# Kernel optimization log

Measured on AMD Instinct MI355X. Metric: run time of the kernel, lower is better.

Reference implementation:

```python
import jax, jax.numpy as jnp
import numpy as np

N = 50000      # query points
N0 = 50000     # support points
M = 32         # neighbors per query
K = 15         # kernel points
DIM = 3
D_IN = 64
D_OUT = 64
POINT_INFLUENCE = 1.0
KERNEL_RADIUS = 1.5 * POINT_INFLUENCE  # _INFLUENCE_TO_RADIUS * point_influence


def setup_inputs() -> dict:
    key = jax.random.key(0)
    k1, k2, k3, k4, k5 = jax.random.split(key, 5)
    query_points = jax.random.normal(k1, (N, DIM), jnp.float32)
    support_points = jax.random.normal(k2, (N0, DIM), jnp.float32)
    neighbors = jax.random.randint(k3, (N, M), 0, N0 + 1)  # index N0 = shadow point
    x = jax.random.normal(k4, (N0, D_IN), jnp.float32)
    # Kernel point dispositions: fixed center point, rest spread within kernel radius
    # (stand-in for kernel_point_optimization_debug; K_points is a frozen parameter).
    rng = np.random.RandomState(0)
    kp = rng.uniform(-1.0, 1.0, (K, DIM))
    kp[0, :] = 0.0
    kp = kp * (KERNEL_RADIUS / np.max(np.linalg.norm(kp, axis=1)))
    K_points = jnp.asarray(kp, dtype=jnp.float32)
    # Xavier-normal conv weights [K, D_IN, D_OUT]
    std = (2.0 / (D_IN + D_OUT)) ** 0.5
    weight = jax.random.normal(k5, (K, D_IN, D_OUT), jnp.float32) * std
    return {
        "query_points": query_points,
        "support_points": support_points,
        "neighbors": neighbors,
        "x": x,
        "K_points": K_points,
        "weight": weight,
    }


def reference(query_points, support_points, neighbors, x, K_points, weight):
    # Shadow support point far away + zero shadow feature row
    shadow = jnp.full((1, query_points.shape[1]), 1e6, dtype=support_points.dtype)
    sp = jnp.concatenate([support_points, shadow], axis=0)            # [N0+1, 3]
    xp = jnp.concatenate([x, jnp.zeros((1, x.shape[1]), x.dtype)], axis=0)  # [N0+1, d]

    # Gather neighbor coords, center on query point
    neighb_pts = sp[neighbors] - query_points[:, None, :]             # [N, M, 3]
    # Squared distances to each kernel point
    diff = neighb_pts[:, :, None, :] - K_points[None, None, :, :]     # [N, M, K, 3]
    sq_distances = jnp.sum(diff * diff, axis=-1)                      # [N, M, K]

    # Linear influence, then transpose to [N, K, M]
    all_weights = jnp.clip(1.0 - jnp.sqrt(sq_distances) / POINT_INFLUENCE, 0.0)
    all_weights = jnp.swapaxes(all_weights, 1, 2)                     # [N, K, M]

    # Gather neighbor features and aggregate per kernel point
    feats = xp[neighbors]                                             # [N, M, d]
    weighted = jnp.einsum("nkm,nmd->nkd", all_weights, feats)        # [N, K, d]
    # Apply per-kernel-point weight matrices and sum over kernel points
    out = jnp.einsum("nkd,kdo->no", weighted, weight)                # [N, out]
    return out
```

## Files before the change

### kernel.cpp

```cpp
#include <hip/hip_runtime.h>

#define NQ 50000
#define NS 50000
#define MNB 32
#define KP 15
#define QPB 32
#define NBLK 1563

typedef __bf16 bf16x8 __attribute__((ext_vector_type(8)));
typedef float  f32x4  __attribute__((ext_vector_type(4)));

__device__ __forceinline__ unsigned short bf1(float f) {
    union { __bf16 h; unsigned short s; } r; r.h = (__bf16)f; return r.s;
}
__device__ __forceinline__ unsigned pk2(float a, float b) {
    union { __bf16 h[2]; unsigned u; } r;
    r.h[0] = (__bf16)a; r.h[1] = (__bf16)b; return r.u;
}

#define PERM_LO 0x05040100u
#define PERM_HI 0x07060302u

__global__ __launch_bounds__(256) void conv_prep(const float* __restrict__ W,
                                                 uint4* __restrict__ wBf,
                                                 const float* __restrict__ x,
                                                 uint4* __restrict__ xBf) {
    const int b = blockIdx.x;
    if (b < 32) {
        const int c = b * 256 + threadIdx.x;
        const int cl = c & 15, qq = (c >> 4) & 3, ks = (c >> 6) & 31, cc = c >> 11;
        const int k0 = ks * 32 + qq * 8;
        const int o  = cc * 16 + cl;
        union { unsigned short s[8]; uint4 u; } pk;
        #pragma unroll
        for (int j = 0; j < 8; ++j)
            pk.s[j] = (k0 + j < KP * 64) ? bf1(W[(size_t)(k0 + j) * 64 + o])
                                         : (unsigned short)0;
        wBf[c] = pk.u;
    } else {
        const int t = (b - 32) * 256 + threadIdx.x;
        if (t < (NS * 64) / 8) {
            const float4* __restrict__ x4 = (const float4*)x;
            const float4 a = x4[t * 2];
            const float4 c2 = x4[t * 2 + 1];
            uint4 o;
            o.x = pk2(a.x, a.y);  o.y = pk2(a.z, a.w);
            o.z = pk2(c2.x, c2.y); o.w = pk2(c2.z, c2.w);
            xBf[t] = o;
        }
    }
}

__global__ __launch_bounds__(1024, 8) void kpconv_fused(
    const float* __restrict__ qp, const float* __restrict__ sp,
    const int* __restrict__ nb, const uint2* __restrict__ xb,
    const float* __restrict__ kpts, const uint4* __restrict__ wBf,
    float* __restrict__ out)
{
    __shared__ struct {
        __align__(16) unsigned short wt[QPB * 1024];
        union {
            float4 rc4[QPB][MNB];
            f32x4  red[8][64];
        } u;
    } sm;

    const int tid  = threadIdx.x;
    const int lane = tid & 63;
    const int wv   = __builtin_amdgcn_readfirstlane(tid >> 6);
    const int cl = lane & 15, q = lane >> 4;
    const int n0 = blockIdx.x * QPB;

    const int   kidx = (cl < KP) ? cl : (KP - 1);
    const float kx = kpts[kidx * 3 + 0];
    const float ky = kpts[kidx * 3 + 1];
    const float kz = kpts[kidx * 3 + 2];
    const float gate = (cl < KP) ? 1.0f : 0.0f;

    {
        const int m  = lane & 31, gh = lane >> 5;
        const int n  = n0 + wv * 2 + gh;
        float rx = 1e6f, ry = 1e6f, rz = 1e6f; int idc = 0;
        if (n < NQ) {
            const int id = nb[n * MNB + m];
            const float qx = qp[n * 3 + 0], qy = qp[n * 3 + 1], qz = qp[n * 3 + 2];
            float sx = 1e6f, sy = 1e6f, sz = 1e6f;
            if (id < NS) { sx = sp[id*3+0]; sy = sp[id*3+1]; sz = sp[id*3+2]; }
            rx = sx - qx; ry = sy - qy; rz = sz - qz;
            idc = (id < NS) ? id : 0;
        }
        sm.u.rc4[wv * 2 + gh][m] = (float4){rx, ry, rz, __int_as_float(idc)};
    }

    const f32x4 zero = (f32x4){0.f, 0.f, 0.f, 0.f};
    #pragma unroll 1
    for (int gg = 0; gg < 2; ++gg) {
        const int g = wv * 2 + gg;
        float w[8]; uint2 r[8];
        #pragma unroll
        for (int j = 0; j < 8; ++j) {
            const float4 rc = sm.u.rc4[g][4 * j + q];
            const float dx = rc.x - kx, dy = rc.y - ky, dz = rc.z - kz;
            const float d2 = dx * dx + dy * dy + dz * dz;
            w[j] = fmaxf(1.0f - __builtin_amdgcn_sqrtf(d2), 0.0f) * gate;
            r[j] = xb[(size_t)__float_as_uint(rc.w) * 16 + cl];
        }
        union { uint4 u; bf16x8 v; } wf;
        wf.u.x = pk2(w[0], w[1]); wf.u.y = pk2(w[2], w[3]);
        wf.u.z = pk2(w[4], w[5]); wf.u.w = pk2(w[6], w[7]);
        union { uint4 u; bf16x8 v; } af[4];
        #pragma unroll
        for (int pr = 0; pr < 4; ++pr) {
            const uint2 e = r[2 * pr], o = r[2 * pr + 1];
            ((unsigned*)&af[0].u)[pr] = __builtin_amdgcn_perm(o.x, e.x, PERM_LO);
            ((unsigned*)&af[1].u)[pr] = __builtin_amdgcn_perm(o.x, e.x, PERM_HI);
            ((unsigned*)&af[2].u)[pr] = __builtin_amdgcn_perm(o.y, e.y, PERM_LO);
            ((unsigned*)&af[3].u)[pr] = __builtin_amdgcn_perm(o.y, e.y, PERM_HI);
        }
        f32x4 acc[4];
        #pragma unroll
        for (int cb = 0; cb < 4; ++cb)
            acc[cb] = __builtin_amdgcn_mfma_f32_16x16x32_bf16(af[cb].v, wf.v, zero, 0, 0, 0);
        unsigned pkd[8];
        #pragma unroll
        for (int i = 0; i < 4; ++i) {
            pkd[2 * i]     = pk2(acc[0][i], acc[1][i]);
            pkd[2 * i + 1] = pk2(acc[2][i], acc[3][i]);
        }
        const unsigned key = (unsigned)(((g & 7) ^ (cl & 7)) << 4);
        char* base = (char*)sm.wt + g * 2048;
        const unsigned i0 = (unsigned)(cl * 128 + q * 32);
        *(uint4*)(base + ((i0)      ^ key)) = (uint4){pkd[0], pkd[1], pkd[2], pkd[3]};
        *(uint4*)(base + ((i0 + 16) ^ key)) = (uint4){pkd[4], pkd[5], pkd[6], pkd[7]};
    }

    __syncthreads();

    const int h  = wv >> 3;
    const int tl = wv & 7;
    const int rc = tl >> 2, cc = tl & 3;
    const char* abase = (const char*)sm.wt + (rc * 16 + cl) * 2048;
    const unsigned akey = (unsigned)((cl & 7) << 4);
    const uint4* wb = wBf + (((cc * 32 + h * 16) * 4 + q) * 16 + cl);
    f32x4 d0 = zero, d1 = zero;
    #pragma unroll 4
    for (int it = 0; it < 16; it += 2) {
        const int ks0 = h * 16 + it;
        const unsigned kk  = (unsigned)((((ks0 >> 1) & 7)) << 4);
        const unsigned ia0 = (unsigned)(ks0 * 64 + q * 16);
        const bf16x8 a0 = *(const bf16x8*)(abase + ((ia0)      ^ akey ^ kk));
        const bf16x8 a1 = *(const bf16x8*)(abase + ((ia0 + 64) ^ akey ^ kk));
        union { uint4 u; bf16x8 v; } b0, b1;
        b0.u = wb[it * 64];
        b1.u = wb[it * 64 + 64];
        d0 = __builtin_amdgcn_mfma_f32_16x16x32_bf16(a0, b0.v, d0, 0, 0, 0);
        d1 = __builtin_amdgcn_mfma_f32_16x16x32_bf16(a1, b1.v, d1, 0, 0, 0);
    }
    f32x4 dd = d0 + d1;
    if (h == 1) sm.u.red[tl][lane] = dd;
    __syncthreads();
    if (h == 0) {
        dd += sm.u.red[tl][lane];
        #pragma unroll
        for (int i = 0; i < 4; ++i) {
            const int n = n0 + rc * 16 + q * 4 + i;
            if (n < NQ) out[(size_t)n * 64 + cc * 16 + cl] = dd[i];
        }
    }
}

extern "C" void kernel_launch(void* const* d_in, const int* in_sizes, int n_in,
                              void* d_out, int out_size, void* d_ws, size_t ws_size,
                              hipStream_t stream) {
    const float* qp   = (const float*)d_in[0];
    const float* sp   = (const float*)d_in[1];
    const int*   nb   = (const int*)d_in[2];
    const float* x    = (const float*)d_in[3];
    const float* kpts = (const float*)d_in[4];
    const float* W    = (const float*)d_in[5];
    float* out = (float*)d_out;

    uint4* wBf = (uint4*)d_ws;
    uint4* xBf = (uint4*)((char*)d_ws + 131072);

    hipLaunchKernelGGL(conv_prep, dim3(32 + (NS * 64 / 8 + 255) / 256), dim3(256),
                       0, stream, W, wBf, x, xBf);
    hipLaunchKernelGGL(kpconv_fused, dim3(NBLK), dim3(1024), 0, stream,
                       qp, sp, nb, (const uint2*)xBf, kpts, wBf, out);
}
```

Before: 122.5 us.

## Pad shadow row in prep and gather neighbors directly without LDS staging

The prep kernel now writes padded copies of the support coordinates and bf16 features, with a shadow row at index NS (coordinates 1e6, features zero). The fused kernel can then gather coordinates and features straight from global memory per MFMA lane, with no shadow-index branch and no LDS staging of relative coordinates. Each lane now reloads coordinates and the neighbor index itself (redundantly across its 16 column lanes), and the query offset is folded into the kernel-point position. Nontemporal hints are added on the neighbor loads and output stores.

```diff
diff --git a/kernel.cpp b/kernel.cpp
--- a/kernel.cpp
+++ b/kernel.cpp
@@ -6,6 +6,10 @@
 #define KP 15
 #define QPB 32
 #define NBLK 1563
+
+#define WBF_BYTES 131072
+#define XBF_BYTES ((NS + 1) * 128)
+#define SP2_OFF   (WBF_BYTES + XBF_BYTES)
 
 typedef __bf16 bf16x8 __attribute__((ext_vector_type(8)));
 typedef float  f32x4  __attribute__((ext_vector_type(4)));
@@ -24,7 +28,9 @@
 __global__ __launch_bounds__(256) void conv_prep(const float* __restrict__ W,
                                                  uint4* __restrict__ wBf,
                                                  const float* __restrict__ x,
-                                                 uint4* __restrict__ xBf) {
+                                                 uint4* __restrict__ xBf,
+                                                 const float* __restrict__ sp,
+                                                 float* __restrict__ sp2) {
     const int b = blockIdx.x;
     if (b < 32) {
         const int c = b * 256 + threadIdx.x;
@@ -37,7 +43,7 @@
             pk.s[j] = (k0 + j < KP * 64) ? bf1(W[(size_t)(k0 + j) * 64 + o])
                                          : (unsigned short)0;
         wBf[c] = pk.u;
-    } else {
+    } else if (b < 1595) {
         const int t = (b - 32) * 256 + threadIdx.x;
         if (t < (NS * 64) / 8) {
             const float4* __restrict__ x4 = (const float4*)x;
@@ -47,22 +53,25 @@
             o.x = pk2(a.x, a.y);  o.y = pk2(a.z, a.w);
             o.z = pk2(c2.x, c2.y); o.w = pk2(c2.z, c2.w);
             xBf[t] = o;
+        } else if (t < (NS * 64) / 8 + 8) {
+            xBf[t] = (uint4){0u, 0u, 0u, 0u};
         }
+    } else {
+        const int i = (b - 1595) * 256 + threadIdx.x;
+        if (i < (NS + 1) * 3)
+            sp2[i] = (i < NS * 3) ? sp[i] : 1e6f;
     }
 }
 
 __global__ __launch_bounds__(1024, 8) void kpconv_fused(
-    const float* __restrict__ qp, const float* __restrict__ sp,
+    const float* __restrict__ qp, const float* __restrict__ sp2,
     const int* __restrict__ nb, const uint2* __restrict__ xb,
     const float* __restrict__ kpts, const uint4* __restrict__ wBf,
     float* __restrict__ out)
 {
     __shared__ struct {
         __align__(16) unsigned short wt[QPB * 1024];
-        union {
-            float4 rc4[QPB][MNB];
-            f32x4  red[8][64];
-        } u;
+        __align__(16) f32x4 red[8][64];
     } sm;
 
     const int tid  = threadIdx.x;
@@ -71,40 +80,37 @@
     const int cl = lane & 15, q = lane >> 4;
     const int n0 = blockIdx.x * QPB;
 
-    const int   kidx = (cl < KP) ? cl : (KP - 1);
-    const float kx = kpts[kidx * 3 + 0];
-    const float ky = kpts[kidx * 3 + 1];
-    const float kz = kpts[kidx * 3 + 2];
-    const float gate = (cl < KP) ? 1.0f : 0.0f;
-
-    {
-        const int m  = lane & 31, gh = lane >> 5;
-        const int n  = n0 + wv * 2 + gh;
-        float rx = 1e6f, ry = 1e6f, rz = 1e6f; int idc = 0;
-        if (n < NQ) {
-            const int id = nb[n * MNB + m];
-            const float qx = qp[n * 3 + 0], qy = qp[n * 3 + 1], qz = qp[n * 3 + 2];
-            float sx = 1e6f, sy = 1e6f, sz = 1e6f;
-            if (id < NS) { sx = sp[id*3+0]; sy = sp[id*3+1]; sz = sp[id*3+2]; }
-            rx = sx - qx; ry = sy - qy; rz = sz - qz;
-            idc = (id < NS) ? id : 0;
-        }
-        sm.u.rc4[wv * 2 + gh][m] = (float4){rx, ry, rz, __int_as_float(idc)};
-    }
+    const float kx = (cl < KP) ? kpts[cl * 3 + 0] : 1e9f;
+    const float ky = (cl < KP) ? kpts[cl * 3 + 1] : 1e9f;
+    const float kz = (cl < KP) ? kpts[cl * 3 + 2] : 1e9f;
 
     const f32x4 zero = (f32x4){0.f, 0.f, 0.f, 0.f};
+
     #pragma unroll 1
     for (int gg = 0; gg < 2; ++gg) {
         const int g = wv * 2 + gg;
+        const int n = n0 + g;
+        const int nc = (n < NQ) ? n : (NQ - 1);
+        const float qx = qp[nc * 3 + 0];
+        const float qy = qp[nc * 3 + 1];
+        const float qz = qp[nc * 3 + 2];
+        const float kqx = kx + qx, kqy = ky + qy, kqz = kz + qz;
+        const int* __restrict__ nbq = nb + nc * MNB;
+
         float w[8]; uint2 r[8];
         #pragma unroll
         for (int j = 0; j < 8; ++j) {
-            const float4 rc = sm.u.rc4[g][4 * j + q];
-            const float dx = rc.x - kx, dy = rc.y - ky, dz = rc.z - kz;
+            const unsigned id = (unsigned)__builtin_nontemporal_load(&nbq[4 * j + q]);
+            const unsigned so = id * 3u;
+            const float sx = sp2[so + 0];
+            const float sy = sp2[so + 1];
+            const float sz = sp2[so + 2];
+            r[j] = xb[id * 16u + (unsigned)cl];
+            const float dx = sx - kqx, dy = sy - kqy, dz = sz - kqz;
             const float d2 = dx * dx + dy * dy + dz * dz;
-            w[j] = fmaxf(1.0f - __builtin_amdgcn_sqrtf(d2), 0.0f) * gate;
-            r[j] = xb[(size_t)__float_as_uint(rc.w) * 16 + cl];
+            w[j] = fmaxf(1.0f - __builtin_amdgcn_sqrtf(d2), 0.0f);
         }
+
         union { uint4 u; bf16x8 v; } wf;
         wf.u.x = pk2(w[0], w[1]); wf.u.y = pk2(w[2], w[3]);
         wf.u.z = pk2(w[4], w[5]); wf.u.w = pk2(w[6], w[7]);
@@ -157,14 +163,15 @@
         d1 = __builtin_amdgcn_mfma_f32_16x16x32_bf16(a1, b1.v, d1, 0, 0, 0);
     }
     f32x4 dd = d0 + d1;
-    if (h == 1) sm.u.red[tl][lane] = dd;
+    if (h == 1) sm.red[tl][lane] = dd;
     __syncthreads();
     if (h == 0) {
-        dd += sm.u.red[tl][lane];
+        dd += sm.red[tl][lane];
         #pragma unroll
         for (int i = 0; i < 4; ++i) {
             const int n = n0 + rc * 16 + q * 4 + i;
-            if (n < NQ) out[(size_t)n * 64 + cc * 16 + cl] = dd[i];
+            if (n < NQ)
+                __builtin_nontemporal_store(dd[i], &out[(size_t)n * 64 + cc * 16 + cl]);
         }
     }
 }
@@ -181,10 +188,12 @@
     float* out = (float*)d_out;
 
     uint4* wBf = (uint4*)d_ws;
-    uint4* xBf = (uint4*)((char*)d_ws + 131072);
+    uint4* xBf = (uint4*)((char*)d_ws + WBF_BYTES);
+    float* sp2 = (float*)((char*)d_ws + SP2_OFF);
 
-    hipLaunchKernelGGL(conv_prep, dim3(32 + (NS * 64 / 8 + 255) / 256), dim3(256),
-                       0, stream, W, wBf, x, xBf);
+    const int spBlocks = ((NS + 1) * 3 + 255) / 256;
+    hipLaunchKernelGGL(conv_prep, dim3(1595 + spBlocks), dim3(256), 0, stream,
+                       W, wBf, x, xBf, sp, sp2);
     hipLaunchKernelGGL(kpconv_fused, dim3(NBLK), dim3(1024), 0, stream,
-                       qp, sp, nb, (const uint2*)xBf, kpts, wBf, out);
+                       qp, sp2, nb, (const uint2*)xBf, kpts, wBf, out);
 }
```

Measured after the change: 138.9 us. +13.4%, slower.
